# Kernel tuning notes

Measured on AMD Instinct MI355X. Metric: run time of the kernel, lower is better.

Reference implementation:

```python
import jax, jax.numpy as jnp
import numpy as np

N_NODES = 50000
N_EDGES = 600000
N_GRAPHS = 64


def _linear_init(key, fan_in, fan_out):
    # torch nn.Linear default: U(-1/sqrt(fan_in), 1/sqrt(fan_in))
    s = 1.0 / np.sqrt(fan_in)
    kw, kb = jax.random.split(key)
    W = jax.random.uniform(kw, (fan_in, fan_out), jnp.float32, -s, s)
    b = jax.random.uniform(kb, (fan_out,), jnp.float32, -s, s)
    return W, b


def setup_inputs() -> dict:
    key = jax.random.key(0)
    ks = jax.random.split(key, 7)
    x = jax.random.normal(ks[0], (N_NODES, 128), jnp.float32)
    edge_index = jax.random.randint(ks[1], (2, N_EDGES), 0, N_NODES, dtype=jnp.int32).astype(jnp.int64)
    batch = jnp.sort(jax.random.randint(ks[2], (N_NODES,), 0, N_GRAPHS, dtype=jnp.int32)).astype(jnp.int64)
    W1, b1 = _linear_init(ks[3], 128, 256)
    W2, b2 = _linear_init(ks[4], 256, 256)
    W3, b3 = _linear_init(ks[5], 256, 128)
    W4, b4 = _linear_init(ks[6], 128, 10)
    return dict(x=x, edge_index=edge_index, batch=batch,
                W1=W1, b1=b1, W2=W2, b2=b2, W3=W3, b3=b3, W4=W4, b4=b4)


def _gcn_conv(h, src, dst, W, b, n_nodes):
    # PyG GCNConv: add self-loops (src/dst already include them),
    # symmetric normalization D^{-1/2} (A+I) D^{-1/2} h W + b.
    h = h @ W                                      # [N, Cout]
    deg = jax.ops.segment_sum(jnp.ones(src.shape[0], h.dtype), dst, num_segments=n_nodes)
    dinv = jnp.where(deg > 0, jax.lax.rsqrt(deg), 0.0)
    norm = dinv[src] * dinv[dst]                   # [E+N]
    msg = h[src] * norm[:, None]                   # gather + scale per edge
    agg = jax.ops.segment_sum(msg, dst, num_segments=n_nodes)  # scatter-add
    return agg + b


def reference(x, edge_index, batch, W1, b1, W2, b2, W3, b3, W4, b4):
    n = x.shape[0]
    loops = jnp.arange(n, dtype=edge_index.dtype)
    src = jnp.concatenate([edge_index[0], loops])
    dst = jnp.concatenate([edge_index[1], loops])
    # GCNBlock (activate_last=True since dense layers follow)
    h = jax.nn.relu(_gcn_conv(x, src, dst, W1, b1, n))
    h = jax.nn.relu(_gcn_conv(h, src, dst, W2, b2, n))
    # global_mean_pool over batch segments
    sums = jax.ops.segment_sum(h, batch, num_segments=N_GRAPHS)          # [G, 256]
    counts = jax.ops.segment_sum(jnp.ones((n,), h.dtype), batch, num_segments=N_GRAPHS)
    g = sums / jnp.maximum(counts, 1.0)[:, None]
    # DenseBlock [256 -> 128 -> 10], activate_last=False
    g = jax.nn.relu(g @ W3 + b3)
    return g @ W4 + b4
```

## Files before the change

### kernel.cpp

```cpp
#include <hip/hip_runtime.h>

typedef unsigned short u16;
typedef unsigned int u32;
typedef __attribute__((ext_vector_type(8))) short s16x8;
typedef __attribute__((ext_vector_type(4))) float f32x4;

#define NN 50000
#define NE 600000
#define NG 64

__device__ __forceinline__ u16 f2bf(float f) {
    u32 u = __float_as_uint(f);
    u32 r = (u + 0x7fffu + ((u >> 16) & 1u)) >> 16;
    return (u16)r;
}
__device__ __forceinline__ float bf2f(u16 h) {
    return __uint_as_float(((u32)h) << 16);
}
__device__ __forceinline__ void gll16(const void* g, void* l) {
    __builtin_amdgcn_global_load_lds((const __attribute__((address_space(1))) u32*)g,
                                     (__attribute__((address_space(3))) u32*)l, 16, 0, 0);
}

__global__ void k_hist(const int* __restrict__ dst, int* __restrict__ cnt, int ne) {
    int e = blockIdx.x * blockDim.x + threadIdx.x;
    if (e < ne) atomicAdd(&cnt[dst[e]], 1);
}

__global__ __launch_bounds__(256)
void k_scan1(const int* __restrict__ cnt, int* __restrict__ bsum, int n) {
    int i = blockIdx.x * 256 + threadIdx.x;
    int v = (i < n) ? cnt[i] : 0;
#pragma unroll
    for (int off = 32; off > 0; off >>= 1) v += __shfl_down(v, off, 64);
    __shared__ int ws[4];
    int lane = threadIdx.x & 63, w = threadIdx.x >> 6;
    if (lane == 0) ws[w] = v;
    __syncthreads();
    if (threadIdx.x == 0) bsum[blockIdx.x] = ws[0] + ws[1] + ws[2] + ws[3];
}

__global__ __launch_bounds__(256)
void k_scan2(int* __restrict__ bsum, int nb) {
    int t = threadIdx.x;
    int v = (t < nb) ? bsum[t] : 0;
    int lane = t & 63, w = t >> 6;
    int inc = v;
#pragma unroll
    for (int off = 1; off < 64; off <<= 1) {
        int x = __shfl_up(inc, off, 64);
        if (lane >= off) inc += x;
    }
    __shared__ int wtot[4];
    if (lane == 63) wtot[w] = inc;
    __syncthreads();
    int wo = 0;
    for (int j = 0; j < w; ++j) wo += wtot[j];
    if (t < nb) bsum[t] = wo + inc - v;
}

__global__ __launch_bounds__(256)
void k_scan3(const int* __restrict__ cnt, const int* __restrict__ boff,
             int* __restrict__ rowptr, int* __restrict__ cursor,
             float* __restrict__ dinv, int n) {
    int i = blockIdx.x * 256 + threadIdx.x;
    int v = (i < n) ? cnt[i] : 0;
    int lane = threadIdx.x & 63, w = threadIdx.x >> 6;
    int inc = v;
#pragma unroll
    for (int off = 1; off < 64; off <<= 1) {
        int x = __shfl_up(inc, off, 64);
        if (lane >= off) inc += x;
    }
    __shared__ int wtot[4];
    if (lane == 63) wtot[w] = inc;
    __syncthreads();
    int wo = boff[blockIdx.x];
    for (int j = 0; j < w; ++j) wo += wtot[j];
    if (i < n) {
        int excl = wo + inc - v;
        rowptr[i] = excl;
        cursor[i] = excl;
        dinv[i] = rsqrtf(1.0f + (float)v);
        if (i == n - 1) rowptr[n] = excl + v;
    }
}

__global__ void k_fill(const int* __restrict__ src, const int* __restrict__ dst,
                       int* __restrict__ cursor, int* __restrict__ csr_src, int ne) {
    int e = blockIdx.x * blockDim.x + threadIdx.x;
    if (e < ne) {
        int pos = atomicAdd(&cursor[dst[e]], 1);
        csr_src[pos] = src[e];
    }
}

__device__ __forceinline__ void wsplit_tiled(const float* __restrict__ W,
                                             u16* __restrict__ hi, int gid) {
    int n = gid & 255, kgrp = gid >> 8;
    int kbase = kgrp * 8;
#pragma unroll
    for (int j = 0; j < 8; ++j) {
        float w = W[(size_t)(kbase + j) * 256 + n];
        hi[(size_t)gid * 8 + j] = f2bf(w);
    }
}

__global__ __launch_bounds__(256)
void k_preamble(const float* __restrict__ x, u16* __restrict__ xbf,
                const float* __restrict__ W1, u16* __restrict__ w1hi,
                const float* __restrict__ W2, u16* __restrict__ w2hi,
                float* __restrict__ sums, int* __restrict__ cnt,
                const int* __restrict__ batch, float* __restrict__ counts) {
    const int XB = (NN * 32 + 255) / 256;
    const int CB = (NN + 255) / 256;
    int b = blockIdx.x, t = threadIdx.x;
    if (b < XB) {
        int i = b * 256 + t;
        if (i < NN * 32) {
            float4 v = ((const float4*)x)[i];
            ushort4 o;
            o.x = f2bf(v.x); o.y = f2bf(v.y); o.z = f2bf(v.z); o.w = f2bf(v.w);
            ((ushort4*)xbf)[i] = o;
        }
        return;
    }
    b -= XB;
    if (b < 16) { wsplit_tiled(W1, w1hi, b * 256 + t); return; }
    b -= 16;
    if (b < 32) { wsplit_tiled(W2, w2hi, b * 256 + t); return; }
    b -= 32;
    if (b < 64) { sums[b * 256 + t] = 0.f; return; }
    b -= 64;
    if (b < CB) {
        int i = b * 256 + t;
        if (i < NN) cnt[i] = 0;
        return;
    }
    b -= CB;
    if (b == 0) {
        __shared__ int lb[65];
        if (t <= 64) {
            int lo = 0, hi = NN;
            while (lo < hi) {
                int mid = (lo + hi) >> 1;
                if (batch[mid] < t) lo = mid + 1; else hi = mid;
            }
            lb[t] = lo;
        }
        __syncthreads();
        if (t < 64) counts[t] = (float)(lb[t + 1] - lb[t]);
    }
}

__device__ __forceinline__ void fma8(float* a, const uint4& v, float w) {
    a[0] += bf2f((u16)v.x) * w; a[1] += bf2f((u16)(v.x >> 16)) * w;
    a[2] += bf2f((u16)v.y) * w; a[3] += bf2f((u16)(v.y >> 16)) * w;
    a[4] += bf2f((u16)v.z) * w; a[5] += bf2f((u16)(v.z >> 16)) * w;
    a[6] += bf2f((u16)v.w) * w; a[7] += bf2f((u16)(v.w >> 16)) * w;
}
__device__ __forceinline__ void fma4(float* a, const uint2& v, float w) {
    a[0] += bf2f((u16)v.x) * w; a[1] += bf2f((u16)(v.x >> 16)) * w;
    a[2] += bf2f((u16)v.y) * w; a[3] += bf2f((u16)(v.y >> 16)) * w;
}

template<int C>
__global__ __launch_bounds__(256)
void k_agg_gather(const int* __restrict__ rowptr, const int* __restrict__ csr_src,
                  const float* __restrict__ dinv, const u16* __restrict__ hb,
                  u16* __restrict__ out, int n) {
    constexpr int VL = C / 32;
    int tid = threadIdx.x;
    int node = (blockIdx.x * 256 + tid) >> 5;
    if (node >= n) return;
    int sl = tid & 31;
    int hbase = tid & 32;
    int beg = rowptr[node], end = rowptr[node + 1];
    int m = end - beg;
    float di = dinv[node];
    float a0[VL], a1[VL];
    if constexpr (VL == 8) {
        uint4 v = ((const uint4*)hb)[(size_t)node * 32 + sl];
#pragma unroll
        for (int i = 0; i < 8; ++i) a1[i] = 0.f;
        a0[0] = bf2f((u16)v.x) * di; a0[1] = bf2f((u16)(v.x >> 16)) * di;
        a0[2] = bf2f((u16)v.y) * di; a0[3] = bf2f((u16)(v.y >> 16)) * di;
        a0[4] = bf2f((u16)v.z) * di; a0[5] = bf2f((u16)(v.z >> 16)) * di;
        a0[6] = bf2f((u16)v.w) * di; a0[7] = bf2f((u16)(v.w >> 16)) * di;
    } else {
        uint2 v = ((const uint2*)hb)[(size_t)node * 32 + sl];
#pragma unroll
        for (int i = 0; i < 4; ++i) a1[i] = 0.f;
        a0[0] = bf2f((u16)v.x) * di; a0[1] = bf2f((u16)(v.x >> 16)) * di;
        a0[2] = bf2f((u16)v.y) * di; a0[3] = bf2f((u16)(v.y >> 16)) * di;
    }
    for (int base = 0; base < m; base += 32) {
        int c = m - base; if (c > 32) c = 32;
        int sid = 0; float w = 0.f;
        if (sl < c) { sid = csr_src[beg + base + sl]; w = dinv[sid]; }
        int cr = (c + 3) & ~3;
        for (int e = 0; e < cr; e += 4) {
            int   s0 = __shfl(sid, hbase + e, 64),     s1 = __shfl(sid, hbase + e + 1, 64);
            int   s2 = __shfl(sid, hbase + e + 2, 64), s3 = __shfl(sid, hbase + e + 3, 64);
            float w0 = __shfl(w, hbase + e, 64),       w1 = __shfl(w, hbase + e + 1, 64);
            float w2 = __shfl(w, hbase + e + 2, 64),   w3 = __shfl(w, hbase + e + 3, 64);
            if constexpr (VL == 8) {
                uint4 r0 = ((const uint4*)hb)[(size_t)s0 * 32 + sl];
                uint4 r1 = ((const uint4*)hb)[(size_t)s1 * 32 + sl];
                uint4 r2 = ((const uint4*)hb)[(size_t)s2 * 32 + sl];
                uint4 r3 = ((const uint4*)hb)[(size_t)s3 * 32 + sl];
                fma8(a0, r0, w0); fma8(a1, r1, w1); fma8(a0, r2, w2); fma8(a1, r3, w3);
            } else {
                uint2 r0 = ((const uint2*)hb)[(size_t)s0 * 32 + sl];
                uint2 r1 = ((const uint2*)hb)[(size_t)s1 * 32 + sl];
                uint2 r2 = ((const uint2*)hb)[(size_t)s2 * 32 + sl];
                uint2 r3 = ((const uint2*)hb)[(size_t)s3 * 32 + sl];
                fma4(a0, r0, w0); fma4(a1, r1, w1); fma4(a0, r2, w2); fma4(a1, r3, w3);
            }
        }
    }
    if constexpr (VL == 8) {
        uint4 o;
        o.x = (u32)f2bf((a0[0] + a1[0]) * di) | ((u32)f2bf((a0[1] + a1[1]) * di) << 16);
        o.y = (u32)f2bf((a0[2] + a1[2]) * di) | ((u32)f2bf((a0[3] + a1[3]) * di) << 16);
        o.z = (u32)f2bf((a0[4] + a1[4]) * di) | ((u32)f2bf((a0[5] + a1[5]) * di) << 16);
        o.w = (u32)f2bf((a0[6] + a1[6]) * di) | ((u32)f2bf((a0[7] + a1[7]) * di) << 16);
        ((uint4*)out)[(size_t)node * 32 + sl] = o;
    } else {
        uint2 o;
        o.x = (u32)f2bf((a0[0] + a1[0]) * di) | ((u32)f2bf((a0[1] + a1[1]) * di) << 16);
        o.y = (u32)f2bf((a0[2] + a1[2]) * di) | ((u32)f2bf((a0[3] + a1[3]) * di) << 16);
        ((uint2*)out)[(size_t)node * 32 + sl] = o;
    }
}

template<bool POOL>
__global__ __launch_bounds__(512, 4)
void k_gemm_mfma(const u16* __restrict__ A, const u16* __restrict__ Bh,
                 const float* __restrict__ bias, u16* __restrict__ out_bf,
                 const int* __restrict__ batch, float* __restrict__ pool,
                 int M, int K) {
    __shared__ u16 ldsA[2][4096];
    const int tid = threadIdx.x, lane = tid & 63, wid = tid >> 6;
    const int bm = blockIdx.x * 128;
    const int wr = (wid >> 2) * 64, wc = (wid & 3) * 64;
    const int lr = lane & 15, kg = lane >> 4;

    const int srow = wid * 16 + (lane >> 2);
    const int sslot = lane & 3;
    const int ssw = (srow ^ (srow >> 2)) & 3;
    int srg = bm + srow; if (srg >= M) srg = M - 1;
    const u16* sbase = A + (size_t)srg * K + ((sslot ^ ssw) << 3);

    const u16* bh_p = Bh + (u32)kg * 2048 + (u32)(wc + lr) * 8;

    f32x4 acc[4][4];
#pragma unroll
    for (int i = 0; i < 4; ++i)
#pragma unroll
        for (int j = 0; j < 4; ++j) acc[i][j] = (f32x4){0.f, 0.f, 0.f, 0.f};

    const int nt = K >> 5;
    gll16(sbase, &ldsA[0][wid * 512]);
    __syncthreads();

    for (int t = 0; t < nt; ++t) {
        int cur = t & 1;
        if (t + 1 < nt)
            gll16(sbase + ((t + 1) << 5), &ldsA[cur ^ 1][wid * 512]);

        s16x8 bh[4];
#pragma unroll
        for (int fn = 0; fn < 4; ++fn)
            bh[fn] = *(const s16x8*)&bh_p[(u32)t * 8192 + (u32)fn * 128];
        const u16* lb = ldsA[cur];
        s16x8 a[4];
#pragma unroll
        for (int fm = 0; fm < 4; ++fm) {
            int r = wr + fm * 16 + lr;
            a[fm] = *(const s16x8*)&lb[r * 32 + ((kg ^ ((r ^ (r >> 2)) & 3)) << 3)];
        }
#pragma unroll
        for (int fn = 0; fn < 4; ++fn)
#pragma unroll
            for (int fm = 0; fm < 4; ++fm)
                acc[fm][fn] = __builtin_amdgcn_mfma_f32_16x16x32_bf16(a[fm], bh[fn], acc[fm][fn], 0, 0, 0);
        __syncthreads();
    }

#pragma unroll
    for (int fn = 0; fn < 4; ++fn) {
        int col = wc + fn * 16 + lr;
        float bv = bias[col];
        if (!POOL) {
#pragma unroll
            for (int fm = 0; fm < 4; ++fm) {
                int rbase = bm + wr + fm * 16 + kg * 4;
#pragma unroll
                for (int r = 0; r < 4; ++r) {
                    int row = rbase + r;
                    if (row < M)
                        out_bf[(size_t)row * 256 + col] = f2bf(fmaxf(acc[fm][fn][r] + bv, 0.f));
                }
            }
        } else {
            int gcur = -1;
            float run = 0.f;
#pragma unroll
            for (int fm = 0; fm < 4; ++fm) {
                int rbase = bm + wr + fm * 16 + kg * 4;
#pragma unroll
                for (int r = 0; r < 4; ++r) {
                    int row = rbase + r;
                    if (row < M) {
                        int g = batch[row];
                        float v = fmaxf(acc[fm][fn][r] + bv, 0.f);
                        if (g != gcur) {
                            if (gcur >= 0) atomicAdd(&pool[gcur * 256 + col], run);
                            gcur = g;
                            run = 0.f;
                        }
                        run += v;
                    }
                }
            }
            if (gcur >= 0) atomicAdd(&pool[gcur * 256 + col], run);
        }
    }
}

__global__ __launch_bounds__(128)
void k_dense(const float* __restrict__ sums, const float* __restrict__ counts,
             const float* __restrict__ W3, const float* __restrict__ b3,
             const float* __restrict__ W4, const float* __restrict__ b4,
             float* __restrict__ out) {
    __shared__ float g[256];
    __shared__ float hid[128];
    int gi = blockIdx.x;
    int t = threadIdx.x;
    float inv = 1.0f / fmaxf(counts[gi], 1.0f);
    for (int c = t; c < 256; c += 128) g[c] = sums[gi * 256 + c] * inv;
    __syncthreads();
    float acc = b3[t];
    for (int k = 0; k < 256; ++k) acc += g[k] * W3[k * 128 + t];
    hid[t] = fmaxf(acc, 0.0f);
    __syncthreads();
    if (t < 10) {
        float o = b4[t];
        for (int k = 0; k < 128; ++k) o += hid[k] * W4[k * 10 + t];
        out[gi * 10 + t] = o;
    }
}

extern "C" void kernel_launch(void* const* d_in, const int* in_sizes, int n_in,
                              void* d_out, int out_size, void* d_ws, size_t ws_size,
                              hipStream_t stream) {
    const float* x   = (const float*)d_in[0];
    const int*  eidx = (const int*)d_in[1];
    const int*  batch= (const int*)d_in[2];
    const float* W1 = (const float*)d_in[3];
    const float* b1 = (const float*)d_in[4];
    const float* W2 = (const float*)d_in[5];
    const float* b2 = (const float*)d_in[6];
    const float* W3 = (const float*)d_in[7];
    const float* b3 = (const float*)d_in[8];
    const float* W4 = (const float*)d_in[9];
    const float* b4 = (const float*)d_in[10];
    float* out = (float*)d_out;

    const int N = NN, E = NE, G = NG;
    const int* src = eidx;
    const int* dst = eidx + E;
    const int NB = (N + 255) / 256;

    char* p = (char*)d_ws;
    auto alloc = [&](size_t bytes) { char* r = p; p += (bytes + 255) & ~(size_t)255; return r; };
    u16*   h1bf   = (u16*)alloc((size_t)N * 256 * 2);
    u16*   xbf    = (u16*)alloc((size_t)N * 128 * 2);
    float* dinv   = (float*)alloc((size_t)N * 4);
    float* sums   = (float*)alloc((size_t)G * 256 * 4);
    float* counts = (float*)alloc((size_t)G * 4);
    int*   cnt    = (int*)alloc((size_t)N * 4);
    int*   rowptr = (int*)alloc((size_t)(N + 1) * 4);
    int*   bsum   = (int*)alloc((size_t)NB * 4);
    int*   csr    = (int*)alloc((size_t)E * 4);
    u16*   agg1   = (u16*)alloc((size_t)N * 128 * 2);
    u16*   agg2   = (u16*)alloc((size_t)N * 256 * 2);
    u16*   w1hi   = (u16*)alloc((size_t)256 * 128 * 2);
    u16*   w2hi   = (u16*)alloc((size_t)256 * 256 * 2);
    int*   cursor = cnt;

    const int XB = (NN * 32 + 255) / 256;
    const int CB = (NN + 255) / 256;
    int pre_blocks = XB + 16 + 32 + 64 + CB + 1;
    k_preamble<<<pre_blocks, 256, 0, stream>>>(x, xbf, W1, w1hi, W2, w2hi,
                                               sums, cnt, batch, counts);

    k_hist<<<(E + 255) / 256, 256, 0, stream>>>(dst, cnt, E);
    k_scan1<<<NB, 256, 0, stream>>>(cnt, bsum, N);
    k_scan2<<<1, 256, 0, stream>>>(bsum, NB);
    k_scan3<<<NB, 256, 0, stream>>>(cnt, bsum, rowptr, cursor, dinv, N);
    k_fill<<<(E + 255) / 256, 256, 0, stream>>>(src, dst, cursor, csr, E);

    k_agg_gather<128><<<(N + 7) / 8, 256, 0, stream>>>(rowptr, csr, dinv, xbf, agg1, N);
    int gblocks = (N + 127) / 128;
    k_gemm_mfma<false><<<gblocks, 512, 0, stream>>>(agg1, w1hi, b1, h1bf,
                                                    nullptr, nullptr, N, 128);

    k_agg_gather<256><<<(N + 7) / 8, 256, 0, stream>>>(rowptr, csr, dinv, h1bf, agg2, N);
    k_gemm_mfma<true><<<gblocks, 512, 0, stream>>>(agg2, w2hi, b2, nullptr,
                                                   batch, sums, N, 256);

    k_dense<<<G, 128, 0, stream>>>(sums, counts, W3, b3, W4, b4, out);
}
```

Measured before the change: 213.6 us.

## Slice feature layout by 32-column chunks and pack edge weights into CSR

Stores node features (x in bf16 and the layer-1 output) in a column-sliced layout where each 32-feature slice of all nodes is contiguous. Aggregation runs one slice per block group, so the gathered working set per slice is smaller and may stay resident in L2. The CSR now stores (src, dinv[src]) pairs so the aggregation avoids a dependent dinv lookup per edge. The cost is many more blocks, a narrower 4-byte load per lane per edge, and repeated reads of CSR and rowptr once per slice.

```diff
diff --git a/kernel.cpp b/kernel.cpp
--- a/kernel.cpp
+++ b/kernel.cpp
@@ -87,11 +87,13 @@
 }
 
 __global__ void k_fill(const int* __restrict__ src, const int* __restrict__ dst,
-                       int* __restrict__ cursor, int* __restrict__ csr_src, int ne) {
+                       const float* __restrict__ dinv,
+                       int* __restrict__ cursor, uint2* __restrict__ csr2, int ne) {
     int e = blockIdx.x * blockDim.x + threadIdx.x;
     if (e < ne) {
         int pos = atomicAdd(&cursor[dst[e]], 1);
-        csr_src[pos] = src[e];
+        int s = src[e];
+        csr2[pos] = make_uint2((u32)s, __float_as_uint(dinv[s]));
     }
 }
 
@@ -107,7 +109,7 @@
 }
 
 __global__ __launch_bounds__(256)
-void k_preamble(const float* __restrict__ x, u16* __restrict__ xbf,
+void k_preamble(const float* __restrict__ x, u16* __restrict__ xbf_s,
                 const float* __restrict__ W1, u16* __restrict__ w1hi,
                 const float* __restrict__ W2, u16* __restrict__ w2hi,
                 float* __restrict__ sums, int* __restrict__ cnt,
@@ -119,9 +121,14 @@
         int i = b * 256 + t;
         if (i < NN * 32) {
             float4 v = ((const float4*)x)[i];
-            ushort4 o;
-            o.x = f2bf(v.x); o.y = f2bf(v.y); o.z = f2bf(v.z); o.w = f2bf(v.w);
-            ((ushort4*)xbf)[i] = o;
+            int node = i >> 5;
+            int q = i & 31;
+            int slice = q >> 3;
+            int uoff = (q & 7) * 2;
+            uint2 o;
+            o.x = (u32)f2bf(v.x) | ((u32)f2bf(v.y) << 16);
+            o.y = (u32)f2bf(v.z) | ((u32)f2bf(v.w) << 16);
+            ((uint2*)xbf_s)[(((size_t)slice * NN + node) * 16 + uoff) >> 1] = o;
         }
         return;
     }
@@ -153,85 +160,59 @@
     }
 }
 
-__device__ __forceinline__ void fma8(float* a, const uint4& v, float w) {
-    a[0] += bf2f((u16)v.x) * w; a[1] += bf2f((u16)(v.x >> 16)) * w;
-    a[2] += bf2f((u16)v.y) * w; a[3] += bf2f((u16)(v.y >> 16)) * w;
-    a[4] += bf2f((u16)v.z) * w; a[5] += bf2f((u16)(v.z >> 16)) * w;
-    a[6] += bf2f((u16)v.w) * w; a[7] += bf2f((u16)(v.w >> 16)) * w;
-}
-__device__ __forceinline__ void fma4(float* a, const uint2& v, float w) {
-    a[0] += bf2f((u16)v.x) * w; a[1] += bf2f((u16)(v.x >> 16)) * w;
-    a[2] += bf2f((u16)v.y) * w; a[3] += bf2f((u16)(v.y >> 16)) * w;
-}
-
 template<int C>
 __global__ __launch_bounds__(256)
-void k_agg_gather(const int* __restrict__ rowptr, const int* __restrict__ csr_src,
-                  const float* __restrict__ dinv, const u16* __restrict__ hb,
+void k_agg_sliced(const int* __restrict__ rowptr, const uint2* __restrict__ csr2,
+                  const float* __restrict__ dinv, const u16* __restrict__ hbs,
                   u16* __restrict__ out, int n) {
-    constexpr int VL = C / 32;
-    int tid = threadIdx.x;
-    int node = (blockIdx.x * 256 + tid) >> 5;
-    if (node >= n) return;
-    int sl = tid & 31;
-    int hbase = tid & 32;
+    constexpr int NS = C / 32;
+    const int nodeblocks = (NN + 15) / 16;
+    int slice = blockIdx.x / nodeblocks;
+    int nb = blockIdx.x - slice * nodeblocks;
+    int lane = threadIdx.x & 63, wave = threadIdx.x >> 6;
+    int g = lane >> 4, li = lane & 15;
+    int node = nb * 16 + wave * 4 + g;
+    if (node >= n) node = n - 1;
     int beg = rowptr[node], end = rowptr[node + 1];
     int m = end - beg;
     float di = dinv[node];
-    float a0[VL], a1[VL];
-    if constexpr (VL == 8) {
-        uint4 v = ((const uint4*)hb)[(size_t)node * 32 + sl];
-#pragma unroll
-        for (int i = 0; i < 8; ++i) a1[i] = 0.f;
-        a0[0] = bf2f((u16)v.x) * di; a0[1] = bf2f((u16)(v.x >> 16)) * di;
-        a0[2] = bf2f((u16)v.y) * di; a0[3] = bf2f((u16)(v.y >> 16)) * di;
-        a0[4] = bf2f((u16)v.z) * di; a0[5] = bf2f((u16)(v.z >> 16)) * di;
-        a0[6] = bf2f((u16)v.w) * di; a0[7] = bf2f((u16)(v.w >> 16)) * di;
-    } else {
-        uint2 v = ((const uint2*)hb)[(size_t)node * 32 + sl];
-#pragma unroll
-        for (int i = 0; i < 4; ++i) a1[i] = 0.f;
-        a0[0] = bf2f((u16)v.x) * di; a0[1] = bf2f((u16)(v.x >> 16)) * di;
-        a0[2] = bf2f((u16)v.y) * di; a0[3] = bf2f((u16)(v.y >> 16)) * di;
-    }
-    for (int base = 0; base < m; base += 32) {
-        int c = m - base; if (c > 32) c = 32;
-        int sid = 0; float w = 0.f;
-        if (sl < c) { sid = csr_src[beg + base + sl]; w = dinv[sid]; }
-        int cr = (c + 3) & ~3;
-        for (int e = 0; e < cr; e += 4) {
-            int   s0 = __shfl(sid, hbase + e, 64),     s1 = __shfl(sid, hbase + e + 1, 64);
-            int   s2 = __shfl(sid, hbase + e + 2, 64), s3 = __shfl(sid, hbase + e + 3, 64);
-            float w0 = __shfl(w, hbase + e, 64),       w1 = __shfl(w, hbase + e + 1, 64);
-            float w2 = __shfl(w, hbase + e + 2, 64),   w3 = __shfl(w, hbase + e + 3, 64);
-            if constexpr (VL == 8) {
-                uint4 r0 = ((const uint4*)hb)[(size_t)s0 * 32 + sl];
-                uint4 r1 = ((const uint4*)hb)[(size_t)s1 * 32 + sl];
-                uint4 r2 = ((const uint4*)hb)[(size_t)s2 * 32 + sl];
-                uint4 r3 = ((const uint4*)hb)[(size_t)s3 * 32 + sl];
-                fma8(a0, r0, w0); fma8(a1, r1, w1); fma8(a0, r2, w2); fma8(a1, r3, w3);
-            } else {
-                uint2 r0 = ((const uint2*)hb)[(size_t)s0 * 32 + sl];
-                uint2 r1 = ((const uint2*)hb)[(size_t)s1 * 32 + sl];
-                uint2 r2 = ((const uint2*)hb)[(size_t)s2 * 32 + sl];
-                uint2 r3 = ((const uint2*)hb)[(size_t)s3 * 32 + sl];
-                fma4(a0, r0, w0); fma4(a1, r1, w1); fma4(a0, r2, w2); fma4(a1, r3, w3);
-            }
-        }
-    }
-    if constexpr (VL == 8) {
-        uint4 o;
-        o.x = (u32)f2bf((a0[0] + a1[0]) * di) | ((u32)f2bf((a0[1] + a1[1]) * di) << 16);
-        o.y = (u32)f2bf((a0[2] + a1[2]) * di) | ((u32)f2bf((a0[3] + a1[3]) * di) << 16);
-        o.z = (u32)f2bf((a0[4] + a1[4]) * di) | ((u32)f2bf((a0[5] + a1[5]) * di) << 16);
-        o.w = (u32)f2bf((a0[6] + a1[6]) * di) | ((u32)f2bf((a0[7] + a1[7]) * di) << 16);
-        ((uint4*)out)[(size_t)node * 32 + sl] = o;
-    } else {
-        uint2 o;
-        o.x = (u32)f2bf((a0[0] + a1[0]) * di) | ((u32)f2bf((a0[1] + a1[1]) * di) << 16);
-        o.y = (u32)f2bf((a0[2] + a1[2]) * di) | ((u32)f2bf((a0[3] + a1[3]) * di) << 16);
-        ((uint2*)out)[(size_t)node * 32 + sl] = o;
-    }
+    const u32* sb = (const u32*)hbs + (size_t)slice * n * 16;
+
+    u32 v = sb[(size_t)node * 16 + li];
+    float a0 = bf2f((u16)v) * di, b0 = bf2f((u16)(v >> 16)) * di;
+    float a1 = 0.f, b1 = 0.f;
+
+    int mmax = m;
+    mmax = max(mmax, __shfl_xor(mmax, 16, 64));
+    mmax = max(mmax, __shfl_xor(mmax, 32, 64));
+
+    for (int base = 0; base < mmax; base += 16) {
+        int c = m - base;
+        uint2 ew = make_uint2(0u, 0u);
+        if (li < c) ew = csr2[beg + base + li];
+        int t16 = mmax - base; if (t16 > 16) t16 = 16;
+        int gb = lane & 48;
+        for (int e = 0; e + 1 < t16; e += 2) {
+            int   s0 = __shfl((int)ew.x, gb + e, 64);
+            float w0 = __uint_as_float(__shfl((int)ew.y, gb + e, 64));
+            int   s1 = __shfl((int)ew.x, gb + e + 1, 64);
+            float w1 = __uint_as_float(__shfl((int)ew.y, gb + e + 1, 64));
+            u32 r0 = sb[(size_t)s0 * 16 + li];
+            u32 r1 = sb[(size_t)s1 * 16 + li];
+            a0 += bf2f((u16)r0) * w0; b0 += bf2f((u16)(r0 >> 16)) * w0;
+            a1 += bf2f((u16)r1) * w1; b1 += bf2f((u16)(r1 >> 16)) * w1;
+        }
+        if (t16 & 1) {
+            int e = t16 - 1;
+            int   s0 = __shfl((int)ew.x, gb + e, 64);
+            float w0 = __uint_as_float(__shfl((int)ew.y, gb + e, 64));
+            u32 r0 = sb[(size_t)s0 * 16 + li];
+            a0 += bf2f((u16)r0) * w0; b0 += bf2f((u16)(r0 >> 16)) * w0;
+        }
+    }
+    float fa = (a0 + a1) * di, fb = (b0 + b1) * di;
+    u32 o = (u32)f2bf(fa) | ((u32)f2bf(fb) << 16);
+    ((u32*)out)[(((size_t)node * C + slice * 32) >> 1) + li] = o;
 }
 
 template<bool POOL>
@@ -293,6 +274,7 @@
         int col = wc + fn * 16 + lr;
         float bv = bias[col];
         if (!POOL) {
+            size_t sbase_o = ((size_t)(col >> 5) * (size_t)M) * 32 + (col & 31);
 #pragma unroll
             for (int fm = 0; fm < 4; ++fm) {
                 int rbase = bm + wr + fm * 16 + kg * 4;
@@ -300,7 +282,7 @@
                 for (int r = 0; r < 4; ++r) {
                     int row = rbase + r;
                     if (row < M)
-                        out_bf[(size_t)row * 256 + col] = f2bf(fmaxf(acc[fm][fn][r] + bv, 0.f));
+                        out_bf[sbase_o + (size_t)row * 32] = f2bf(fmaxf(acc[fm][fn][r] + bv, 0.f));
                 }
             }
         } else {
@@ -375,15 +357,15 @@
 
     char* p = (char*)d_ws;
     auto alloc = [&](size_t bytes) { char* r = p; p += (bytes + 255) & ~(size_t)255; return r; };
-    u16*   h1bf   = (u16*)alloc((size_t)N * 256 * 2);
-    u16*   xbf    = (u16*)alloc((size_t)N * 128 * 2);
+    u16*   h1bf_s = (u16*)alloc((size_t)N * 256 * 2);
+    u16*   xbf_s  = (u16*)alloc((size_t)N * 128 * 2);
     float* dinv   = (float*)alloc((size_t)N * 4);
     float* sums   = (float*)alloc((size_t)G * 256 * 4);
     float* counts = (float*)alloc((size_t)G * 4);
     int*   cnt    = (int*)alloc((size_t)N * 4);
     int*   rowptr = (int*)alloc((size_t)(N + 1) * 4);
     int*   bsum   = (int*)alloc((size_t)NB * 4);
-    int*   csr    = (int*)alloc((size_t)E * 4);
+    uint2* csr2   = (uint2*)alloc((size_t)E * 8);
     u16*   agg1   = (u16*)alloc((size_t)N * 128 * 2);
     u16*   agg2   = (u16*)alloc((size_t)N * 256 * 2);
     u16*   w1hi   = (u16*)alloc((size_t)256 * 128 * 2);
@@ -393,21 +375,23 @@
     const int XB = (NN * 32 + 255) / 256;
     const int CB = (NN + 255) / 256;
     int pre_blocks = XB + 16 + 32 + 64 + CB + 1;
-    k_preamble<<<pre_blocks, 256, 0, stream>>>(x, xbf, W1, w1hi, W2, w2hi,
+    k_preamble<<<pre_blocks, 256, 0, stream>>>(x, xbf_s, W1, w1hi, W2, w2hi,
                                                sums, cnt, batch, counts);
 
     k_hist<<<(E + 255) / 256, 256, 0, stream>>>(dst, cnt, E);
     k_scan1<<<NB, 256, 0, stream>>>(cnt, bsum, N);
     k_scan2<<<1, 256, 0, stream>>>(bsum, NB);
     k_scan3<<<NB, 256, 0, stream>>>(cnt, bsum, rowptr, cursor, dinv, N);
-    k_fill<<<(E + 255) / 256, 256, 0, stream>>>(src, dst, cursor, csr, E);
-
-    k_agg_gather<128><<<(N + 7) / 8, 256, 0, stream>>>(rowptr, csr, dinv, xbf, agg1, N);
+    k_fill<<<(E + 255) / 256, 256, 0, stream>>>(src, dst, dinv, cursor, csr2, E);
+
+    const int nodeblocks = (N + 15) / 16;
+
+    k_agg_sliced<128><<<4 * nodeblocks, 256, 0, stream>>>(rowptr, csr2, dinv, xbf_s, agg1, N);
     int gblocks = (N + 127) / 128;
-    k_gemm_mfma<false><<<gblocks, 512, 0, stream>>>(agg1, w1hi, b1, h1bf,
+    k_gemm_mfma<false><<<gblocks, 512, 0, stream>>>(agg1, w1hi, b1, h1bf_s,
                                                     nullptr, nullptr, N, 128);
 
-    k_agg_gather<256><<<(N + 7) / 8, 256, 0, stream>>>(rowptr, csr, dinv, h1bf, agg2, N);
+    k_agg_sliced<256><<<8 * nodeblocks, 256, 0, stream>>>(rowptr, csr2, dinv, h1bf_s, agg2, N);
     k_gemm_mfma<true><<<gblocks, 512, 0, stream>>>(agg2, w2hi, b2, nullptr,
                                                    batch, sums, N, 256);
 
```

New measurement: 242.6 us. +13.6%, slower.
